# Kernel tuning notes

Hardware: AMD Instinct MI355X
Metric: run time of the kernel (lower is better)

The kernel has to match this reference:

```python
import jax, jax.numpy as jnp
import numpy as np

B, NP, NR = 4, 2048, 10
EDGE_F = 32
EMB = 64          # emb_features == out_features (required for layer stacking)
ESM_EMB = 64
HEADS = 16
NUM_LAYERS = 4
LN_EPS = 1e-5


def _ln(x, g, b):
    mu = jnp.mean(x, axis=-1, keepdims=True)
    var = jnp.var(x, axis=-1, keepdims=True)
    return (x - mu) / jnp.sqrt(var + LN_EPS) * g + b


def setup_inputs() -> dict:
    key = jax.random.key(0)
    ks = jax.random.split(key, 32)
    s = 0.05  # xavier-ish scale for weights
    inp = {
        "pep_feat": jax.random.normal(ks[0], (B, NP, 27 + 1280), jnp.float32),
        "rec_feat": jax.random.normal(ks[1], (B, NP, NR, 42 + 1280), jnp.float32),
        "edge_feat": jax.random.normal(ks[2], (B, NP, NR, EDGE_F), jnp.float32),
        # embedding weights (torch Linear convention: y = x @ W.T)
        "W_rec_esm": jax.random.normal(ks[3], (ESM_EMB, 1280), jnp.float32) * s,
        "W_pep_esm": jax.random.normal(ks[4], (ESM_EMB, 1280), jnp.float32) * s,
        "W_pep_emb": jax.random.normal(ks[5], (EMB, 27 + ESM_EMB), jnp.float32) * s,
        "W_rec_emb": jax.random.normal(ks[6], (EMB, 21 + ESM_EMB), jnp.float32) * s,
        "W_edge_emb": jax.random.normal(ks[7], (EMB, EDGE_F), jnp.float32) * s,
        "pep_ln_g": jnp.ones((EMB,), jnp.float32),
        "pep_ln_b": jnp.zeros((EMB,), jnp.float32),
        "rec_ln_g": jnp.ones((EMB,), jnp.float32),
        "rec_ln_b": jnp.zeros((EMB,), jnp.float32),
        # stacked GraphAttention layer params [L, ...]
        "ga_Wp": jax.random.normal(ks[8], (NUM_LAYERS, EMB, EMB), jnp.float32) * s,
        "ga_bp": jnp.zeros((NUM_LAYERS, EMB), jnp.float32),
        "ga_Wr": jax.random.normal(ks[9], (NUM_LAYERS, EMB, 2 * EMB), jnp.float32) * s,
        "ga_br": jnp.zeros((NUM_LAYERS, EMB), jnp.float32),
        "ga_Wv": jax.random.normal(ks[10], (NUM_LAYERS, EMB, 2 * EMB), jnp.float32) * s,
        "ga_bv": jnp.zeros((NUM_LAYERS, EMB), jnp.float32),
        # self-attention pooling: LN + MLP [64 -> 64 -> 32 -> 16 heads], no biases
        "pool_ln_g": jnp.ones((EMB,), jnp.float32),
        "pool_ln_b": jnp.zeros((EMB,), jnp.float32),
        "pool_W0": jax.random.normal(ks[11], (EMB, EMB), jnp.float32) * s,
        "pool_W1": jax.random.normal(ks[12], (EMB // 2, EMB), jnp.float32) * s,
        "pool_W2": jax.random.normal(ks[13], (HEADS, EMB // 2), jnp.float32) * s,
        # final projection
        "mlp_W": jax.random.normal(ks[14], (EMB // 2, EMB), jnp.float32) * s,
        "mlp_b": jnp.zeros((EMB // 2,), jnp.float32),
    }
    return inp


def _forward(pep_feat, rec_feat, edge_feat, W_rec_esm, W_pep_esm, W_pep_emb,
             W_rec_emb, W_edge_emb, pep_ln_g, pep_ln_b, rec_ln_g, rec_ln_b,
             ga_Wp, ga_bp, ga_Wr, ga_br, ga_Wv, ga_bv,
             pool_ln_g, pool_ln_b, pool_W0, pool_W1, pool_W2, mlp_W, mlp_b):
    # --- embeddings ---
    rec_esm = rec_feat[..., 42:] @ W_rec_esm.T                       # [B,NP,10,ESM]
    pep_esm = pep_feat[..., -1280:] @ W_pep_esm.T                    # [B,NP,ESM]
    rec = jnp.concatenate([rec_feat[..., :21], rec_esm], axis=-1) @ W_rec_emb.T
    pep = jnp.concatenate([pep_feat[..., :27], pep_esm], axis=-1) @ W_pep_emb.T
    edge = edge_feat @ W_edge_emb.T                                  # [B,NP,10,EMB]
    pep = _ln(pep, pep_ln_g, pep_ln_b)
    rec = _ln(rec, rec_ln_g, rec_ln_b)

    inv_sqrt_d = 1.0 / np.sqrt(EMB).astype(np.float32)
    rec_edge = jnp.concatenate([rec, edge], axis=-1)                 # [B,NP,10,2*EMB]
    # --- stacked GraphAttention layers (dropout = eval-mode identity) ---
    for l in range(NUM_LAYERS):
        q = pep @ ga_Wp[l].T + ga_bp[l]                              # [B,NP,EMB]
        key = rec_edge @ ga_Wr[l].T + ga_br[l]                       # [B,NP,10,EMB]
        val = rec_edge @ ga_Wv[l].T + ga_bv[l]                       # [B,NP,10,EMB]
        logit = jnp.einsum('bpd,bprd->bpr', q, key) * inv_sqrt_d     # [B,NP,10]
        attn = jax.nn.softmax(logit, axis=-1)
        pep = q + jnp.einsum('bpr,bprd->bpd', attn, val)             # [B,NP,EMB]

    # --- self-attention pooling (note: softmax applied twice, as in source) ---
    d = _ln(pep, pool_ln_g, pool_ln_b)                               # [B,NP,EMB]
    h = jnp.tanh(d @ pool_W0.T)
    h = jnp.tanh(h @ pool_W1.T)
    logits = h @ pool_W2.T                                           # [B,NP,HEADS]
    a = jax.nn.softmax(logits, axis=1)
    a = jax.nn.softmax(a, axis=1)
    attended = jnp.einsum('bsh,bsd->bhd', a, d)                      # [B,HEADS,EMB]
    pooled = attended.mean(axis=1)                                   # [B,EMB]
    return pooled @ mlp_W.T + mlp_b                                  # [B,EMB//2]


def reference(pep_feat, rec_feat, edge_feat, W_rec_esm, W_pep_esm, W_pep_emb,
              W_rec_emb, W_edge_emb, pep_ln_g, pep_ln_b, rec_ln_g, rec_ln_b,
              ga_Wp, ga_bp, ga_Wr, ga_br, ga_Wv, ga_bv,
              pool_ln_g, pool_ln_b, pool_W0, pool_W1, pool_W2, mlp_W, mlp_b):
    return _forward(pep_feat, rec_feat, edge_feat, W_rec_esm, W_pep_esm, W_pep_emb,
                    W_rec_emb, W_edge_emb, pep_ln_g, pep_ln_b, rec_ln_g, rec_ln_b,
                    ga_Wp, ga_bp, ga_Wr, ga_br, ga_Wv, ga_bv,
                    pool_ln_g, pool_ln_b, pool_W0, pool_W1, pool_W2, mlp_W, mlp_b)
```

## Files before the change

### kernel.cpp

```cpp
#include <hip/hip_runtime.h>
#include <hip/hip_bf16.h>


typedef __attribute__((ext_vector_type(8))) short bf16x8;
typedef __attribute__((ext_vector_type(4))) float f32x4;

#define MFMA(a, b, c) __builtin_amdgcn_mfma_f32_16x16x32_bf16((a), (b), (c), 0, 0, 0)

#define WB_REC_OFF   0
#define WB_PEP_OFF   83968
#define WB_EDGE_OFF  167936
#define WB_P_OFF     169984
#define WB_R_OFF     186368
#define WB_V_OFF     219136
#define WB_W0_OFF    251904
#define WB_W1_OFF    256000
#define WB_W2_OFF    258048
#define WB_TOTAL     258560

__device__ __forceinline__ unsigned short f2bf(float x) {
  __hip_bfloat16 h = __float2bfloat16(x);
  return __builtin_bit_cast(unsigned short, h);
}
__device__ __forceinline__ float bf2f(unsigned short u) {
  unsigned int t = ((unsigned int)u) << 16;
  return __builtin_bit_cast(float, t);
}
__device__ __forceinline__ bf16x8 loadBc(const unsigned short* base, int chunk, int lane) {
  return *(const bf16x8*)(base + ((size_t)chunk * 64 + lane) * 8);
}
__device__ __forceinline__ float tanhf_fast(float x) {
  float e = __expf(2.f * x);
  return 1.f - 2.f / (e + 1.f);
}
__device__ __forceinline__ int swzr(int r) {
  return (r & 1) | (((r >> 1) & 7) << 2);
}

__global__ __launch_bounds__(256) void k_pack(
    const float* __restrict__ Wresm, const float* __restrict__ Wpesm,
    const float* __restrict__ Wre, const float* __restrict__ Wpe,
    const float* __restrict__ Wedge, const float* __restrict__ Wp,
    const float* __restrict__ Wr, const float* __restrict__ Wv,
    const float* __restrict__ W0, const float* __restrict__ W1,
    const float* __restrict__ W2, unsigned short* __restrict__ WB) {
  const int t = blockIdx.x * 256 + threadIdx.x;
  if (t >= WB_TOTAL) return;
  float v = 0.f;
  if (t < WB_EDGE_OFF) {
    bool isPep = (t >= WB_PEP_OFF);
    int u = isPep ? (t - WB_PEP_OFF) : t;
    int j = u & 7, lane = (u >> 3) & 63, n = (u >> 9) & 3, kc = u >> 11;
    int k = kc * 32 + ((lane >> 4) << 3) + j;
    int col = n * 16 + (lane & 15);
    if (kc < 40) {
      const float* wemb = isPep ? (Wpe + col * 91 + 27) : (Wre + col * 85 + 21);
      const float* wesm = isPep ? Wpesm : Wresm;
      float s = 0.f;
#pragma unroll 8
      for (int e = 0; e < 64; ++e) s += wemb[e] * wesm[e * 1280 + k];
      v = s;
    } else {
      int kl = k - 1280;
      if (isPep) v = (kl < 27) ? Wpe[col * 91 + kl] : 0.f;
      else       v = (kl < 21) ? Wre[col * 85 + kl] : 0.f;
    }
  } else if (t < WB_P_OFF) {
    int u = t - WB_EDGE_OFF;
    int j = u & 7, lane = (u >> 3) & 63, n = (u >> 9) & 3;
    v = Wedge[(n * 16 + (lane & 15)) * 32 + ((lane >> 4) << 3) + j];
  } else if (t < WB_R_OFF) {
    int u = t - WB_P_OFF;
    int l = u >> 12, w = u & 4095;
    int j = w & 7, lane = (w >> 3) & 63, n = (w >> 9) & 3, kc = w >> 11;
    int o = kc * 32 + ((lane >> 4) << 3) + j;
    int d = n * 16 + (lane & 15);
    v = Wp[l * 4096 + d * 64 + o];
  } else if (t < WB_V_OFF) {
    int u = t - WB_R_OFF;
    int l = u >> 13, w = u & 8191;
    int j = w & 7, lane = (w >> 3) & 63, c = (w >> 9) & 15;
    int kc = c >> 3, n = c & 7;
    int o = kc * 32 + ((lane >> 4) << 3) + j;
    int k = n * 16 + (lane & 15);
    v = Wr[l * 8192 + o * 128 + k];
  } else if (t < WB_W0_OFF) {
    int u = t - WB_V_OFF;
    int l = u >> 13, w = u & 8191;
    int j = w & 7, lane = (w >> 3) & 63, n = (w >> 9) & 3, kc = w >> 11;
    int k = kc * 32 + ((lane >> 4) << 3) + j;
    int d = n * 16 + (lane & 15);
    v = Wv[l * 8192 + d * 128 + k];
  } else if (t < WB_W1_OFF) {
    int u = t - WB_W0_OFF;
    int j = u & 7, lane = (u >> 3) & 63, c = u >> 9;
    int kc = c >> 2, n = c & 3;
    v = W0[(n * 16 + (lane & 15)) * 64 + kc * 32 + ((lane >> 4) << 3) + j];
  } else if (t < WB_W2_OFF) {
    int u = t - WB_W1_OFF;
    int j = u & 7, lane = (u >> 3) & 63, c = u >> 9;
    int kc = c >> 1, n = c & 1;
    v = W1[(n * 16 + (lane & 15)) * 64 + kc * 32 + ((lane >> 4) << 3) + j];
  } else {
    int u = t - WB_W2_OFF;
    int j = u & 7, lane = (u >> 3) & 63;
    v = W2[(lane & 15) * 32 + ((lane >> 4) << 3) + j];
  }
  WB[t] = f2bf(v);
}

__global__ __launch_bounds__(64) void k_emb(
    const float* __restrict__ rec_feat, const float* __restrict__ edge_feat,
    const float* __restrict__ pep_feat, const unsigned short* __restrict__ WB,
    const float* __restrict__ rec_g, const float* __restrict__ rec_b,
    const float* __restrict__ pep_g, const float* __restrict__ pep_b,
    unsigned short* __restrict__ rec_edge, unsigned short* __restrict__ pep_out) {
  __shared__ float stg[2][16][128];
  const int bid = blockIdx.x;
  const int lane = threadIdx.x;
  const int quad = lane >> 4, lr = lane & 15;
  const bool isPep = (bid >= 5120);
  const int brow = (isPep ? bid - 5120 : bid) * 16;

  const f32x4 fz = {0.f, 0.f, 0.f, 0.f};
  f32x4 acc[4] = {fz, fz, fz, fz};

  auto frag = [&](int buf, int c) -> bf16x8 {
    const int u0 = c * 8 + quad * 2;
    const int s0 = u0 ^ swzr(lr), s1 = (u0 + 1) ^ swzr(lr);
    const float4 f0 = *(const float4*)((const char*)&stg[buf][lr][0] + s0 * 16);
    const float4 f1 = *(const float4*)((const char*)&stg[buf][lr][0] + s1 * 16);
    bf16x8 a;
#pragma unroll
    for (int j = 0; j < 4; ++j) { a[j] = (short)f2bf(f0[j]); a[4 + j] = (short)f2bf(f1[j]); }
    return a;
  };

  if (!isPep) {
    const float* base = rec_feat + (size_t)brow * 1322 + 42;
    float2 ld2[16];
    auto loadg = [&](int g) {
#pragma unroll
      for (int i = 0; i < 16; ++i)
        ld2[i] = *(const float2*)(base + (size_t)i * 1322 + g * 128 + lane * 2);
    };
    auto writeg = [&](int b) {
#pragma unroll
      for (int i = 0; i < 16; ++i) {
        const int su = (lane >> 1) ^ swzr(i);
        *(float2*)((char*)&stg[b][i][0] + su * 16 + (lane & 1) * 8) = ld2[i];
      }
    };
    loadg(0); writeg(0);
    int buf = 0;
    for (int g = 0; g < 10; ++g) {
      bf16x8 bb[16];
#pragma unroll
      for (int m = 0; m < 16; ++m) bb[m] = loadBc(WB + WB_REC_OFF, g * 16 + m, lane);
      if (g < 9) loadg(g + 1);
#pragma unroll
      for (int c = 0; c < 4; ++c) {
        const bf16x8 a = frag(buf, c);
#pragma unroll
        for (int n = 0; n < 4; ++n) acc[n] = MFMA(a, bb[c * 4 + n], acc[n]);
      }
      if (g < 9) writeg(buf ^ 1);
      buf ^= 1;
    }
    {
      const float* p = rec_feat + (size_t)(brow + lr) * 1322 + quad * 8;
      bf16x8 a;
#pragma unroll
      for (int m = 0; m < 4; ++m) {
        const float2 v = *(const float2*)(p + 2 * m);
        a[2 * m] = (short)f2bf(v.x); a[2 * m + 1] = (short)f2bf(v.y);
      }
#pragma unroll
      for (int n = 0; n < 4; ++n)
        acc[n] = MFMA(a, loadBc(WB + WB_REC_OFF, 160 + n, lane), acc[n]);
    }
  } else {
    const float* base = pep_feat + (size_t)brow * 1307 + 27;
    float ldp[32];
    auto loadg = [&](int g) {
#pragma unroll
      for (int i = 0; i < 16; ++i)
#pragma unroll
        for (int ph = 0; ph < 2; ++ph)
          ldp[i * 2 + ph] = base[(size_t)i * 1307 + g * 128 + ph * 64 + lane];
    };
    auto writeg = [&](int b) {
#pragma unroll
      for (int i = 0; i < 16; ++i)
#pragma unroll
        for (int ph = 0; ph < 2; ++ph) {
          const int su = (ph * 16 + (lane >> 2)) ^ swzr(i);
          *((float*)((char*)&stg[b][i][0] + su * 16 + (lane & 3) * 4)) = ldp[i * 2 + ph];
        }
    };
    loadg(0); writeg(0);
    int buf = 0;
    for (int g = 0; g < 10; ++g) {
      bf16x8 bb[16];
#pragma unroll
      for (int m = 0; m < 16; ++m) bb[m] = loadBc(WB + WB_PEP_OFF, g * 16 + m, lane);
      if (g < 9) loadg(g + 1);
#pragma unroll
      for (int c = 0; c < 4; ++c) {
        const bf16x8 a = frag(buf, c);
#pragma unroll
        for (int n = 0; n < 4; ++n) acc[n] = MFMA(a, bb[c * 4 + n], acc[n]);
      }
      if (g < 9) writeg(buf ^ 1);
      buf ^= 1;
    }
    {
      const float* p = pep_feat + (size_t)(brow + lr) * 1307 + quad * 8;
      bf16x8 a;
#pragma unroll
      for (int j = 0; j < 8; ++j) a[j] = (short)f2bf(p[j]);
#pragma unroll
      for (int n = 0; n < 4; ++n)
        acc[n] = MFMA(a, loadBc(WB + WB_PEP_OFF, 160 + n, lane), acc[n]);
    }
  }

  float s[4], sq[4];
#pragma unroll
  for (int i = 0; i < 4; ++i) {
    s[i] = acc[0][i] + acc[1][i] + acc[2][i] + acc[3][i];
    sq[i] = acc[0][i] * acc[0][i] + acc[1][i] * acc[1][i] +
            acc[2][i] * acc[2][i] + acc[3][i] * acc[3][i];
  }
#pragma unroll
  for (int msk = 1; msk < 16; msk <<= 1) {
#pragma unroll
    for (int i = 0; i < 4; ++i) {
      s[i] += __shfl_xor(s[i], msk);
      sq[i] += __shfl_xor(sq[i], msk);
    }
  }
  const float* gp = isPep ? pep_g : rec_g;
  const float* bp = isPep ? pep_b : rec_b;
  float gv[4], bvl[4];
#pragma unroll
  for (int n = 0; n < 4; ++n) { gv[n] = gp[lr + 16 * n]; bvl[n] = bp[lr + 16 * n]; }

  if (!isPep) {
    f32x4 acce[4] = {fz, fz, fz, fz};
    {
      const float* p = edge_feat + (size_t)(brow + lr) * 32 + quad * 8;
      const float4 f0 = *(const float4*)(p);
      const float4 f1 = *(const float4*)(p + 4);
      bf16x8 a;
#pragma unroll
      for (int j = 0; j < 4; ++j) { a[j] = (short)f2bf(f0[j]); a[4 + j] = (short)f2bf(f1[j]); }
#pragma unroll
      for (int n = 0; n < 4; ++n) acce[n] = MFMA(a, loadBc(WB + WB_EDGE_OFF, n, lane), acce[n]);
    }
#pragma unroll
    for (int i = 0; i < 4; ++i) {
      const float mean = s[i] * (1.f / 64.f);
      const float var = sq[i] * (1.f / 64.f) - mean * mean;
      const float rstd = rsqrtf(var + 1e-5f);
      unsigned short* dst = rec_edge + (size_t)(brow + quad * 4 + i) * 128;
#pragma unroll
      for (int n = 0; n < 4; ++n) {
        dst[lr + 16 * n] = f2bf((acc[n][i] - mean) * rstd * gv[n] + bvl[n]);
        dst[64 + lr + 16 * n] = f2bf(acce[n][i]);
      }
    }
  } else {
#pragma unroll
    for (int i = 0; i < 4; ++i) {
      const float mean = s[i] * (1.f / 64.f);
      const float var = sq[i] * (1.f / 64.f) - mean * mean;
      const float rstd = rsqrtf(var + 1e-5f);
      unsigned short* dst = pep_out + (size_t)(brow + quad * 4 + i) * 64;
#pragma unroll
      for (int n = 0; n < 4; ++n)
        dst[lr + 16 * n] = f2bf((acc[n][i] - mean) * rstd * gv[n] + bvl[n]);
    }
  }
}

__global__ __launch_bounds__(64) void k_ga(
    const unsigned short* __restrict__ rec_edge, const unsigned short* __restrict__ pep_bf,
    const unsigned short* __restrict__ WB,
    const float* __restrict__ ga_bp, const float* __restrict__ ga_bv,
    const float* __restrict__ pool_g, const float* __restrict__ pool_b,
    float* __restrict__ dbuf, float* __restrict__ logitsT) {
  __shared__ unsigned short pep_s[1024];
  __shared__ unsigned short q_s[1024];
  __shared__ unsigned short zs[2048];
  __shared__ float bias_s[512];

  const int lane = threadIdx.x;
  const int quad = lane >> 4, lr = lane & 15;
  const int swz = lr & 7;
  const int pbase = blockIdx.x * 16;
  const f32x4 fz = {0.f, 0.f, 0.f, 0.f};

#pragma unroll
  for (int i = 0; i < 4; ++i) {
    int f = lane + 64 * i;
    bias_s[f] = ga_bp[f];
    bias_s[256 + f] = ga_bv[f];
  }
#pragma unroll
  for (int i = 0; i < 2; ++i) {
    const int G = lane + 64 * i;
    const int p = G >> 3, gg = G & 7;
    const bf16x8 v = *(const bf16x8*)(pep_bf + (size_t)(pbase + p) * 64 + gg * 8);
    *(bf16x8*)(pep_s + p * 64 + ((gg ^ (p & 7)) << 3)) = v;
  }

  auto bwrite = [&](unsigned short* buf, int p, int col, unsigned short val) {
    buf[p * 64 + ((((col >> 3)) ^ (p & 7)) << 3) + (col & 7)] = val;
  };
  auto bfrag = [&](const unsigned short* buf, int kc) -> bf16x8 {
    return *(const bf16x8*)(buf + lr * 64 + ((((kc << 2) + quad) ^ swz) << 3));
  };
  const unsigned short* reb = rec_edge + (size_t)(pbase + lr) * 1280 + quad * 8;

  f32x4 pcur[4];
  for (int l = 0; l < 4; ++l) {
    const unsigned short* WBp = WB + WB_P_OFF + l * 4096;
    const unsigned short* WBr = WB + WB_R_OFF + l * 8192;
    const unsigned short* WBv = WB + WB_V_OFF + l * 8192;
    f32x4 qa[4] = {fz, fz, fz, fz};
#pragma unroll
    for (int kc = 0; kc < 2; ++kc) {
      bf16x8 a = bfrag(pep_s, kc);
#pragma unroll
      for (int n = 0; n < 4; ++n) qa[n] = MFMA(a, loadBc(WBp, kc * 4 + n, lane), qa[n]);
    }
#pragma unroll
    for (int n = 0; n < 4; ++n) {
      const float bpv = bias_s[l * 64 + lr + 16 * n];
#pragma unroll
      for (int i = 0; i < 4; ++i) qa[n][i] += bpv;
    }
#pragma unroll
    for (int n = 0; n < 4; ++n)
#pragma unroll
      for (int i = 0; i < 4; ++i)
        bwrite(q_s, quad * 4 + i, lr + 16 * n, f2bf(qa[n][i]));
    const bf16x8 aq0 = bfrag(q_s, 0), aq1 = bfrag(q_s, 1);
    f32x4 za[8] = {fz, fz, fz, fz, fz, fz, fz, fz};
#pragma unroll
    for (int n = 0; n < 8; ++n) za[n] = MFMA(aq0, loadBc(WBr, n, lane), za[n]);
#pragma unroll
    for (int n = 0; n < 8; ++n) za[n] = MFMA(aq1, loadBc(WBr, 8 + n, lane), za[n]);
#pragma unroll
    for (int n = 0; n < 8; ++n)
#pragma unroll
      for (int i = 0; i < 4; ++i) {
        const int p = quad * 4 + i, k = 16 * n + lr;
        zs[p * 128 + ((((k >> 3) ^ (p & 7)) << 3) | (k & 7))] = f2bf(za[n][i]);
      }
    float zf[4][8];
#pragma unroll
    for (int kc = 0; kc < 4; ++kc) {
      const bf16x8 z8 = *(const bf16x8*)(zs + lr * 128 + (((quad + 4 * kc) ^ swz) << 3));
#pragma unroll
      for (int j = 0; j < 8; ++j) zf[kc][j] = bf2f((unsigned short)z8[j]);
    }
    float lg[10];
#pragma unroll 2
    for (int r = 0; r < 10; ++r) {
      float part = 0.f;
#pragma unroll
      for (int kc = 0; kc < 4; ++kc) {
        const bf16x8 rf = *(const bf16x8*)(reb + r * 128 + kc * 32);
#pragma unroll
        for (int j = 0; j < 8; ++j) part += bf2f((unsigned short)rf[j]) * zf[kc][j];
      }
      part += __shfl_xor(part, 16);
      part += __shfl_xor(part, 32);
      lg[r] = part * 0.125f;
    }
    float mx = lg[0];
#pragma unroll
    for (int r = 1; r < 10; ++r) mx = fmaxf(mx, lg[r]);
    float ssum = 0.f;
#pragma unroll
    for (int r = 0; r < 10; ++r) { lg[r] = __expf(lg[r] - mx); ssum += lg[r]; }
    const float inv = 1.f / ssum;
#pragma unroll
    for (int r = 0; r < 10; ++r) lg[r] *= inv;
    float wsacc[4][8] = {};
#pragma unroll 2
    for (int r = 0; r < 10; ++r) {
#pragma unroll
      for (int kc = 0; kc < 4; ++kc) {
        const bf16x8 rf = *(const bf16x8*)(reb + r * 128 + kc * 32);
#pragma unroll
        for (int j = 0; j < 8; ++j)
          wsacc[kc][j] += lg[r] * bf2f((unsigned short)rf[j]);
      }
    }
    bf16x8 wf[4];
#pragma unroll
    for (int kc = 0; kc < 4; ++kc)
#pragma unroll
      for (int j = 0; j < 8; ++j) wf[kc][j] = (short)f2bf(wsacc[kc][j]);
    f32x4 oa[4] = {fz, fz, fz, fz};
#pragma unroll
    for (int kc = 0; kc < 4; ++kc)
#pragma unroll
      for (int n = 0; n < 4; ++n) oa[n] = MFMA(wf[kc], loadBc(WBv, kc * 4 + n, lane), oa[n]);
#pragma unroll
    for (int n = 0; n < 4; ++n) {
      const float bvv = bias_s[256 + l * 64 + lr + 16 * n];
#pragma unroll
      for (int i = 0; i < 4; ++i) pcur[n][i] = qa[n][i] + oa[n][i] + bvv;
    }
#pragma unroll
    for (int n = 0; n < 4; ++n)
#pragma unroll
      for (int i = 0; i < 4; ++i)
        bwrite(pep_s, quad * 4 + i, lr + 16 * n, f2bf(pcur[n][i]));
  }

  {
    float s[4], sq[4];
#pragma unroll
    for (int i = 0; i < 4; ++i) {
      s[i] = pcur[0][i] + pcur[1][i] + pcur[2][i] + pcur[3][i];
      sq[i] = pcur[0][i] * pcur[0][i] + pcur[1][i] * pcur[1][i] +
              pcur[2][i] * pcur[2][i] + pcur[3][i] * pcur[3][i];
    }
#pragma unroll
    for (int msk = 1; msk < 16; msk <<= 1) {
#pragma unroll
      for (int i = 0; i < 4; ++i) {
        s[i] += __shfl_xor(s[i], msk);
        sq[i] += __shfl_xor(sq[i], msk);
      }
    }
    float gv[4], bv2[4];
#pragma unroll
    for (int n = 0; n < 4; ++n) { gv[n] = pool_g[lr + 16 * n]; bv2[n] = pool_b[lr + 16 * n]; }
    f32x4 d[4];
#pragma unroll
    for (int i = 0; i < 4; ++i) {
      const float mean = s[i] * (1.f / 64.f);
      const float var = sq[i] * (1.f / 64.f) - mean * mean;
      const float rstd = rsqrtf(var + 1e-5f);
#pragma unroll
      for (int n = 0; n < 4; ++n) d[n][i] = (pcur[n][i] - mean) * rstd * gv[n] + bv2[n];
    }
    float* zf32 = (float*)zs;
#pragma unroll
    for (int n = 0; n < 4; ++n)
#pragma unroll
      for (int i = 0; i < 4; ++i)
        zf32[(quad * 4 + i) * 64 + lr + 16 * n] = d[n][i];
#pragma unroll
    for (int i = 0; i < 4; ++i) {
      const float4 v = *(const float4*)(&zf32[i * 256 + lane * 4]);
      *(float4*)(dbuf + (size_t)pbase * 64 + i * 256 + lane * 4) = v;
    }
#pragma unroll
    for (int n = 0; n < 4; ++n)
#pragma unroll
      for (int i = 0; i < 4; ++i)
        bwrite(q_s, quad * 4 + i, lr + 16 * n, f2bf(d[n][i]));
    const bf16x8 ad0 = bfrag(q_s, 0), ad1 = bfrag(q_s, 1);
    f32x4 h0[4] = {fz, fz, fz, fz};
#pragma unroll
    for (int n = 0; n < 4; ++n) {
      h0[n] = MFMA(ad0, loadBc(WB + WB_W0_OFF, n, lane), h0[n]);
      h0[n] = MFMA(ad1, loadBc(WB + WB_W0_OFF, 4 + n, lane), h0[n]);
    }
#pragma unroll
    for (int n = 0; n < 4; ++n)
#pragma unroll
      for (int i = 0; i < 4; ++i)
        bwrite(q_s, quad * 4 + i, lr + 16 * n, f2bf(tanhf_fast(h0[n][i])));
    const bf16x8 ah00 = bfrag(q_s, 0), ah01 = bfrag(q_s, 1);
    f32x4 h1[2] = {fz, fz};
#pragma unroll
    for (int n = 0; n < 2; ++n) {
      h1[n] = MFMA(ah00, loadBc(WB + WB_W1_OFF, n, lane), h1[n]);
      h1[n] = MFMA(ah01, loadBc(WB + WB_W1_OFF, 2 + n, lane), h1[n]);
    }
#pragma unroll
    for (int n = 0; n < 2; ++n)
#pragma unroll
      for (int i = 0; i < 4; ++i)
        bwrite(q_s, quad * 4 + i, lr + 16 * n, f2bf(tanhf_fast(h1[n][i])));
    const bf16x8 ah1 = bfrag(q_s, 0);
    f32x4 lac = MFMA(ah1, loadBc(WB + WB_W2_OFF, 0, lane), fz);
    const int b = pbase >> 11, sx0 = pbase & 2047;
#pragma unroll
    for (int i = 0; i < 4; ++i)
      logitsT[(size_t)(b * 16 + lr) * 2048 + sx0 + quad * 4 + i] = lac[i];
  }
}

__global__ __launch_bounds__(256) void k_pool2(
    const float* __restrict__ logitsT, const float* __restrict__ dbuf,
    float* __restrict__ attp) {
  __shared__ float sh[2048];
  __shared__ float red[8];
  __shared__ float part[16][64];
  const int blk = blockIdx.x;
  const int bh = blk >> 2, q = blk & 3;
  const int b = bh >> 4;
  const int tid = threadIdx.x, lane = tid & 63, wid = tid >> 6;
  const float* lrow = logitsT + (size_t)bh * 2048;

  float m = -1e30f;
  for (int sx = tid; sx < 2048; sx += 256) {
    float v = lrow[sx];
    sh[sx] = v;
    m = fmaxf(m, v);
  }
#pragma unroll
  for (int msk = 1; msk < 64; msk <<= 1) m = fmaxf(m, __shfl_xor(m, msk));
  if (lane == 0) red[wid] = m;
  __syncthreads();
  m = fmaxf(fmaxf(red[0], red[1]), fmaxf(red[2], red[3]));

  float s1 = 0.f;
  for (int sx = tid; sx < 2048; sx += 256) {
    float e = __expf(sh[sx] - m);
    sh[sx] = e;
    s1 += e;
  }
#pragma unroll
  for (int msk = 1; msk < 64; msk <<= 1) s1 += __shfl_xor(s1, msk);
  __syncthreads();
  if (lane == 0) red[4 + wid] = s1;
  __syncthreads();
  s1 = red[4] + red[5] + red[6] + red[7];
  const float invS1 = 1.f / s1;

  float s2 = 0.f;
  for (int sx = tid; sx < 2048; sx += 256) {
    float e2 = __expf((sh[sx] - 1.f) * invS1);
    sh[sx] = e2;
    s2 += e2;
  }
#pragma unroll
  for (int msk = 1; msk < 64; msk <<= 1) s2 += __shfl_xor(s2, msk);
  __syncthreads();
  if (lane == 0) red[wid] = s2;
  __syncthreads();
  s2 = red[0] + red[1] + red[2] + red[3];
  const float invS2 = 1.f / s2;

  const int d16 = tid & 15, sxg = tid >> 4;
  float4 a4 = {0.f, 0.f, 0.f, 0.f};
  const float* db = dbuf + (size_t)b * 2048 * 64 + d16 * 4;
#pragma unroll 4
  for (int sx = q * 512 + sxg; sx < (q + 1) * 512; sx += 16) {
    const float w = sh[sx];
    const float4 v = *(const float4*)(db + (size_t)sx * 64);
    a4.x += w * v.x; a4.y += w * v.y; a4.z += w * v.z; a4.w += w * v.w;
  }
  *(float4*)(&part[sxg][d16 * 4]) = a4;
  __syncthreads();
  if (tid < 64) {
    float s = 0.f;
#pragma unroll
    for (int g2 = 0; g2 < 16; ++g2) s += part[g2][tid];
    attp[(size_t)(bh * 4 + q) * 64 + tid] = s * invS2;
  }
}

__global__ __launch_bounds__(256) void k_final(
    const float* __restrict__ attp, const float* __restrict__ W,
    const float* __restrict__ bias, float* __restrict__ out) {
  __shared__ float pooled[4][64];
  const int tid = threadIdx.x;
  {
    const int b = tid >> 6, d = tid & 63;
    float s = 0.f;
#pragma unroll
    for (int hq = 0; hq < 64; ++hq) s += attp[((size_t)b * 64 + hq) * 64 + d];
    pooled[b][d] = s * (1.f / 16.f);
  }
  __syncthreads();
  if (tid < 128) {
    const int b = tid >> 5, j = tid & 31;
    float s = bias[j];
#pragma unroll
    for (int d2 = 0; d2 < 64; ++d2) s += pooled[b][d2] * W[j * 64 + d2];
    out[b * 32 + j] = s;
  }
}

extern "C" void kernel_launch(void* const* d_in, const int* in_sizes, int n_in,
                              void* d_out, int out_size, void* d_ws, size_t ws_size,
                              hipStream_t stream) {
  const float* pep_feat = (const float*)d_in[0];
  const float* rec_feat = (const float*)d_in[1];
  const float* edge_feat = (const float*)d_in[2];
  const float* W_rec_esm = (const float*)d_in[3];
  const float* W_pep_esm = (const float*)d_in[4];
  const float* W_pep_emb = (const float*)d_in[5];
  const float* W_rec_emb = (const float*)d_in[6];
  const float* W_edge_emb = (const float*)d_in[7];
  const float* pep_ln_g = (const float*)d_in[8];
  const float* pep_ln_b = (const float*)d_in[9];
  const float* rec_ln_g = (const float*)d_in[10];
  const float* rec_ln_b = (const float*)d_in[11];
  const float* ga_Wp = (const float*)d_in[12];
  const float* ga_bp = (const float*)d_in[13];
  const float* ga_Wr = (const float*)d_in[14];
  const float* ga_br = (const float*)d_in[15];
  const float* ga_Wv = (const float*)d_in[16];
  const float* ga_bv = (const float*)d_in[17];
  const float* pool_ln_g = (const float*)d_in[18];
  const float* pool_ln_b = (const float*)d_in[19];
  const float* pool_W0 = (const float*)d_in[20];
  const float* pool_W1 = (const float*)d_in[21];
  const float* pool_W2 = (const float*)d_in[22];
  const float* mlp_W = (const float*)d_in[23];
  const float* mlp_b = (const float*)d_in[24];
  float* out = (float*)d_out;
  (void)ga_br;
  (void)ws_size; (void)in_sizes; (void)n_in; (void)out_size;

  char* ws = (char*)d_ws;
  unsigned short* WB = (unsigned short*)(ws);
  unsigned short* rec_edge = (unsigned short*)(ws + 524288);
  unsigned short* pep_bf = (unsigned short*)(ws + 21495808);
  float* dbuf = (float*)(ws + 22544384);
  float* logitsT = (float*)(ws + 24641536);
  float* attp = (float*)(ws + 25165824);

  k_pack<<<1010, 256, 0, stream>>>(W_rec_esm, W_pep_esm, W_rec_emb, W_pep_emb,
                                   W_edge_emb, ga_Wp, ga_Wr, ga_Wv,
                                   pool_W0, pool_W1, pool_W2, WB);
  k_emb<<<5632, 64, 0, stream>>>(rec_feat, edge_feat, pep_feat, WB,
                                 rec_ln_g, rec_ln_b, pep_ln_g, pep_ln_b,
                                 rec_edge, pep_bf);
  k_ga<<<512, 64, 0, stream>>>(rec_edge, pep_bf, WB, ga_bp, ga_bv,
                               pool_ln_g, pool_ln_b, dbuf, logitsT);
  k_pool2<<<256, 256, 0, stream>>>(logitsT, dbuf, attp);
  k_final<<<1, 256, 0, stream>>>(attp, mlp_W, mlp_b, out);
}
```

Measured before the change: 190.9 us.

## Split graph-attention kernel across four waves per 16-peptide block

```diff
diff --git a/kernel.cpp b/kernel.cpp
--- a/kernel.cpp
+++ b/kernel.cpp
@@ -284,7 +284,7 @@
   }
 }
 
-__global__ __launch_bounds__(64) void k_ga(
+__global__ __launch_bounds__(256) void k_ga(
     const unsigned short* __restrict__ rec_edge, const unsigned short* __restrict__ pep_bf,
     const unsigned short* __restrict__ WB,
     const float* __restrict__ ga_bp, const float* __restrict__ ga_bv,
@@ -292,28 +292,34 @@
     float* __restrict__ dbuf, float* __restrict__ logitsT) {
   __shared__ unsigned short pep_s[1024];
   __shared__ unsigned short q_s[1024];
-  __shared__ unsigned short zs[2048];
+  __shared__ __align__(16) unsigned short zs[2048];
   __shared__ float bias_s[512];
-
-  const int lane = threadIdx.x;
+  __shared__ float lgp[4][10][17];
+  __shared__ float redp[4][2][16];
+  __shared__ float oap[4][16][68];
+
+  const int tid = threadIdx.x;
+  const int w = tid >> 6;
+  const int lane = tid & 63;
   const int quad = lane >> 4, lr = lane & 15;
   const int swz = lr & 7;
   const int pbase = blockIdx.x * 16;
+  const int mycol = lr + 16 * w;
   const f32x4 fz = {0.f, 0.f, 0.f, 0.f};
 
-#pragma unroll
-  for (int i = 0; i < 4; ++i) {
-    int f = lane + 64 * i;
-    bias_s[f] = ga_bp[f];
-    bias_s[256 + f] = ga_bv[f];
-  }
-#pragma unroll
-  for (int i = 0; i < 2; ++i) {
-    const int G = lane + 64 * i;
-    const int p = G >> 3, gg = G & 7;
+  bias_s[tid] = ga_bp[tid & 255];
+  bias_s[256 + tid] = ga_bv[tid & 255];
+  if (tid < 128) {
+    const int p = tid >> 3, gg = tid & 7;
     const bf16x8 v = *(const bf16x8*)(pep_bf + (size_t)(pbase + p) * 64 + gg * 8);
     *(bf16x8*)(pep_s + p * 64 + ((gg ^ (p & 7)) << 3)) = v;
   }
+  const unsigned short* reb =
+      rec_edge + (size_t)(pbase + lr) * 1280 + w * 32 + quad * 8;
+  bf16x8 rfs[10];
+#pragma unroll
+  for (int r = 0; r < 10; ++r) rfs[r] = *(const bf16x8*)(reb + r * 128);
+  __syncthreads();
 
   auto bwrite = [&](unsigned short* buf, int p, int col, unsigned short val) {
     buf[p * 64 + ((((col >> 3)) ^ (p & 7)) << 3) + (col & 7)] = val;
@@ -321,65 +327,56 @@
   auto bfrag = [&](const unsigned short* buf, int kc) -> bf16x8 {
     return *(const bf16x8*)(buf + lr * 64 + ((((kc << 2) + quad) ^ swz) << 3));
   };
-  const unsigned short* reb = rec_edge + (size_t)(pbase + lr) * 1280 + quad * 8;
-
-  f32x4 pcur[4];
+
+  f32x4 pcur;
   for (int l = 0; l < 4; ++l) {
     const unsigned short* WBp = WB + WB_P_OFF + l * 4096;
     const unsigned short* WBr = WB + WB_R_OFF + l * 8192;
     const unsigned short* WBv = WB + WB_V_OFF + l * 8192;
-    f32x4 qa[4] = {fz, fz, fz, fz};
-#pragma unroll
-    for (int kc = 0; kc < 2; ++kc) {
-      bf16x8 a = bfrag(pep_s, kc);
-#pragma unroll
-      for (int n = 0; n < 4; ++n) qa[n] = MFMA(a, loadBc(WBp, kc * 4 + n, lane), qa[n]);
-    }
-#pragma unroll
-    for (int n = 0; n < 4; ++n) {
-      const float bpv = bias_s[l * 64 + lr + 16 * n];
-#pragma unroll
-      for (int i = 0; i < 4; ++i) qa[n][i] += bpv;
-    }
-#pragma unroll
-    for (int n = 0; n < 4; ++n)
-#pragma unroll
-      for (int i = 0; i < 4; ++i)
-        bwrite(q_s, quad * 4 + i, lr + 16 * n, f2bf(qa[n][i]));
+
+    f32x4 qa = fz;
+    qa = MFMA(bfrag(pep_s, 0), loadBc(WBp, w, lane), qa);
+    qa = MFMA(bfrag(pep_s, 1), loadBc(WBp, 4 + w, lane), qa);
+    const float bpv = bias_s[l * 64 + mycol];
+#pragma unroll
+    for (int i = 0; i < 4; ++i) qa[i] += bpv;
+#pragma unroll
+    for (int i = 0; i < 4; ++i) bwrite(q_s, quad * 4 + i, mycol, f2bf(qa[i]));
+    __syncthreads();
+
     const bf16x8 aq0 = bfrag(q_s, 0), aq1 = bfrag(q_s, 1);
-    f32x4 za[8] = {fz, fz, fz, fz, fz, fz, fz, fz};
-#pragma unroll
-    for (int n = 0; n < 8; ++n) za[n] = MFMA(aq0, loadBc(WBr, n, lane), za[n]);
-#pragma unroll
-    for (int n = 0; n < 8; ++n) za[n] = MFMA(aq1, loadBc(WBr, 8 + n, lane), za[n]);
-#pragma unroll
-    for (int n = 0; n < 8; ++n)
-#pragma unroll
-      for (int i = 0; i < 4; ++i) {
-        const int p = quad * 4 + i, k = 16 * n + lr;
-        zs[p * 128 + ((((k >> 3) ^ (p & 7)) << 3) | (k & 7))] = f2bf(za[n][i]);
-      }
-    float zf[4][8];
-#pragma unroll
-    for (int kc = 0; kc < 4; ++kc) {
-      const bf16x8 z8 = *(const bf16x8*)(zs + lr * 128 + (((quad + 4 * kc) ^ swz) << 3));
-#pragma unroll
-      for (int j = 0; j < 8; ++j) zf[kc][j] = bf2f((unsigned short)z8[j]);
-    }
-    float lg[10];
-#pragma unroll 2
+    f32x4 za0 = fz, za1 = fz;
+    za0 = MFMA(aq0, loadBc(WBr, 2 * w, lane), za0);
+    za0 = MFMA(aq1, loadBc(WBr, 8 + 2 * w, lane), za0);
+    za1 = MFMA(aq0, loadBc(WBr, 2 * w + 1, lane), za1);
+    za1 = MFMA(aq1, loadBc(WBr, 9 + 2 * w, lane), za1);
+#pragma unroll
+    for (int i = 0; i < 4; ++i) {
+      const int p = quad * 4 + i;
+      const int k0 = 16 * (2 * w) + lr, k1 = 16 * (2 * w + 1) + lr;
+      zs[p * 128 + ((((k0 >> 3) ^ (p & 7)) << 3) | (k0 & 7))] = f2bf(za0[i]);
+      zs[p * 128 + ((((k1 >> 3) ^ (p & 7)) << 3) | (k1 & 7))] = f2bf(za1[i]);
+    }
+    float zfw[8];
+    {
+      const bf16x8 z8 = *(const bf16x8*)(zs + lr * 128 + (((quad + 4 * w) ^ swz) << 3));
+#pragma unroll
+      for (int j = 0; j < 8; ++j) zfw[j] = bf2f((unsigned short)z8[j]);
+    }
+#pragma unroll
     for (int r = 0; r < 10; ++r) {
       float part = 0.f;
 #pragma unroll
-      for (int kc = 0; kc < 4; ++kc) {
-        const bf16x8 rf = *(const bf16x8*)(reb + r * 128 + kc * 32);
-#pragma unroll
-        for (int j = 0; j < 8; ++j) part += bf2f((unsigned short)rf[j]) * zf[kc][j];
-      }
+      for (int j = 0; j < 8; ++j) part += bf2f((unsigned short)rfs[r][j]) * zfw[j];
       part += __shfl_xor(part, 16);
       part += __shfl_xor(part, 32);
-      lg[r] = part * 0.125f;
-    }
+      if (quad == 0) lgp[w][r][lr] = part;
+    }
+    __syncthreads();
+    float lg[10];
+#pragma unroll
+    for (int r = 0; r < 10; ++r)
+      lg[r] = (lgp[0][r][lr] + lgp[1][r][lr] + lgp[2][r][lr] + lgp[3][r][lr]) * 0.125f;
     float mx = lg[0];
 #pragma unroll
     for (int r = 1; r < 10; ++r) mx = fmaxf(mx, lg[r]);
@@ -389,48 +386,41 @@
     const float inv = 1.f / ssum;
 #pragma unroll
     for (int r = 0; r < 10; ++r) lg[r] *= inv;
-    float wsacc[4][8] = {};
-#pragma unroll 2
-    for (int r = 0; r < 10; ++r) {
-#pragma unroll
-      for (int kc = 0; kc < 4; ++kc) {
-        const bf16x8 rf = *(const bf16x8*)(reb + r * 128 + kc * 32);
-#pragma unroll
-        for (int j = 0; j < 8; ++j)
-          wsacc[kc][j] += lg[r] * bf2f((unsigned short)rf[j]);
-      }
-    }
-    bf16x8 wf[4];
-#pragma unroll
-    for (int kc = 0; kc < 4; ++kc)
-#pragma unroll
-      for (int j = 0; j < 8; ++j) wf[kc][j] = (short)f2bf(wsacc[kc][j]);
-    f32x4 oa[4] = {fz, fz, fz, fz};
-#pragma unroll
-    for (int kc = 0; kc < 4; ++kc)
-#pragma unroll
-      for (int n = 0; n < 4; ++n) oa[n] = MFMA(wf[kc], loadBc(WBv, kc * 4 + n, lane), oa[n]);
-#pragma unroll
-    for (int n = 0; n < 4; ++n) {
-      const float bvv = bias_s[256 + l * 64 + lr + 16 * n];
-#pragma unroll
-      for (int i = 0; i < 4; ++i) pcur[n][i] = qa[n][i] + oa[n][i] + bvv;
-    }
+    float wsacc[8] = {};
+#pragma unroll
+    for (int r = 0; r < 10; ++r)
+#pragma unroll
+      for (int j = 0; j < 8; ++j)
+        wsacc[j] += lg[r] * bf2f((unsigned short)rfs[r][j]);
+    bf16x8 wf;
+#pragma unroll
+    for (int j = 0; j < 8; ++j) wf[j] = (short)f2bf(wsacc[j]);
+    f32x4 oa[4];
+#pragma unroll
+    for (int n = 0; n < 4; ++n) oa[n] = MFMA(wf, loadBc(WBv, w * 4 + n, lane), fz);
 #pragma unroll
     for (int n = 0; n < 4; ++n)
 #pragma unroll
       for (int i = 0; i < 4; ++i)
-        bwrite(pep_s, quad * 4 + i, lr + 16 * n, f2bf(pcur[n][i]));
+        oap[w][quad * 4 + i][n * 16 + lr] = oa[n][i];
+    __syncthreads();
+    const float bvv = bias_s[256 + l * 64 + mycol];
+#pragma unroll
+    for (int i = 0; i < 4; ++i) {
+      const int p = quad * 4 + i;
+      const float o = oap[0][p][mycol] + oap[1][p][mycol] +
+                      oap[2][p][mycol] + oap[3][p][mycol];
+      pcur[i] = qa[i] + o + bvv;
+    }
+#pragma unroll
+    for (int i = 0; i < 4; ++i) bwrite(pep_s, quad * 4 + i, mycol, f2bf(pcur[i]));
+    __syncthreads();
   }
 
   {
     float s[4], sq[4];
 #pragma unroll
-    for (int i = 0; i < 4; ++i) {
-      s[i] = pcur[0][i] + pcur[1][i] + pcur[2][i] + pcur[3][i];
-      sq[i] = pcur[0][i] * pcur[0][i] + pcur[1][i] * pcur[1][i] +
-              pcur[2][i] * pcur[2][i] + pcur[3][i] * pcur[3][i];
-    }
+    for (int i = 0; i < 4; ++i) { s[i] = pcur[i]; sq[i] = pcur[i] * pcur[i]; }
 #pragma unroll
     for (int msk = 1; msk < 16; msk <<= 1) {
 #pragma unroll
@@ -439,64 +429,66 @@
         sq[i] += __shfl_xor(sq[i], msk);
       }
     }
-    float gv[4], bv2[4];
-#pragma unroll
-    for (int n = 0; n < 4; ++n) { gv[n] = pool_g[lr + 16 * n]; bv2[n] = pool_b[lr + 16 * n]; }
-    f32x4 d[4];
+    if (lr == 0) {
+#pragma unroll
+      for (int i = 0; i < 4; ++i) {
+        redp[w][0][quad * 4 + i] = s[i];
+        redp[w][1][quad * 4 + i] = sq[i];
+      }
+    }
+    __syncthreads();
+    const float gv = pool_g[mycol], bv2 = pool_b[mycol];
+    float d[4];
+    float* zf32 = (float*)zs;
 #pragma unroll
     for (int i = 0; i < 4; ++i) {
-      const float mean = s[i] * (1.f / 64.f);
-      const float var = sq[i] * (1.f / 64.f) - mean * mean;
+      const int p = quad * 4 + i;
+      const float sf = redp[0][0][p] + redp[1][0][p] + redp[2][0][p] + redp[3][0][p];
+      const float sqf = redp[0][1][p] + redp[1][1][p] + redp[2][1][p] + redp[3][1][p];
+      const float mean = sf * (1.f / 64.f);
+      const float var = sqf * (1.f / 64.f) - mean * mean;
       const float rstd = rsqrtf(var + 1e-5f);
-#pragma unroll
-      for (int n = 0; n < 4; ++n) d[n][i] = (pcur[n][i] - mean) * rstd * gv[n] + bv2[n];
-    }
-    float* zf32 = (float*)zs;
-#pragma unroll
-    for (int n = 0; n < 4; ++n)
+      d[i] = (pcur[i] - mean) * rstd * gv + bv2;
+      zf32[p * 64 + mycol] = d[i];
+      bwrite(q_s, p, mycol, f2bf(d[i]));
+    }
+    __syncthreads();
+    {
+      const float4 v = *(const float4*)(&zf32[tid * 4]);
+      *(float4*)(dbuf + (size_t)pbase * 64 + tid * 4) = v;
+    }
+    if (w == 0) {
+      const bf16x8 ad0 = bfrag(q_s, 0), ad1 = bfrag(q_s, 1);
+      f32x4 h0[4] = {fz, fz, fz, fz};
+#pragma unroll
+      for (int n = 0; n < 4; ++n) {
+        h0[n] = MFMA(ad0, loadBc(WB + WB_W0_OFF, n, lane), h0[n]);
+        h0[n] = MFMA(ad1, loadBc(WB + WB_W0_OFF, 4 + n, lane), h0[n]);
+      }
+#pragma unroll
+      for (int n = 0; n < 4; ++n)
+#pragma unroll
+        for (int i = 0; i < 4; ++i)
+          bwrite(q_s, quad * 4 + i, lr + 16 * n, f2bf(tanhf_fast(h0[n][i])));
+      const bf16x8 ah00 = bfrag(q_s, 0), ah01 = bfrag(q_s, 1);
+      f32x4 h1[2] = {fz, fz};
+#pragma unroll
+      for (int n = 0; n < 2; ++n) {
+        h1[n] = MFMA(ah00, loadBc(WB + WB_W1_OFF, n, lane), h1[n]);
+        h1[n] = MFMA(ah01, loadBc(WB + WB_W1_OFF, 2 + n, lane), h1[n]);
+      }
+#pragma unroll
+      for (int n = 0; n < 2; ++n)
+#pragma unroll
+        for (int i = 0; i < 4; ++i)
+          bwrite(q_s, quad * 4 + i, lr + 16 * n, f2bf(tanhf_fast(h1[n][i])));
+      const bf16x8 ah1 = bfrag(q_s, 0);
+      f32x4 lac = MFMA(ah1, loadBc(WB + WB_W2_OFF, 0, lane), fz);
+      const int b = pbase >> 11, sx0 = pbase & 2047;
 #pragma unroll
       for (int i = 0; i < 4; ++i)
-        zf32[(quad * 4 + i) * 64 + lr + 16 * n] = d[n][i];
-#pragma unroll
-    for (int i = 0; i < 4; ++i) {
-      const float4 v = *(const float4*)(&zf32[i * 256 + lane * 4]);
-      *(float4*)(dbuf + (size_t)pbase * 64 + i * 256 + lane * 4) = v;
-    }
-#pragma unroll
-    for (int n = 0; n < 4; ++n)
-#pragma unroll
-      for (int i = 0; i < 4; ++i)
-        bwrite(q_s, quad * 4 + i, lr + 16 * n, f2bf(d[n][i]));
-    const bf16x8 ad0 = bfrag(q_s, 0), ad1 = bfrag(q_s, 1);
-    f32x4 h0[4] = {fz, fz, fz, fz};
-#pragma unroll
-    for (int n = 0; n < 4; ++n) {
-      h0[n] = MFMA(ad0, loadBc(WB + WB_W0_OFF, n, lane), h0[n]);
-      h0[n] = MFMA(ad1, loadBc(WB + WB_W0_OFF, 4 + n, lane), h0[n]);
-    }
-#pragma unroll
-    for (int n = 0; n < 4; ++n)
-#pragma unroll
-      for (int i = 0; i < 4; ++i)
-        bwrite(q_s, quad * 4 + i, lr + 16 * n, f2bf(tanhf_fast(h0[n][i])));
-    const bf16x8 ah00 = bfrag(q_s, 0), ah01 = bfrag(q_s, 1);
-    f32x4 h1[2] = {fz, fz};
-#pragma unroll
-    for (int n = 0; n < 2; ++n) {
-      h1[n] = MFMA(ah00, loadBc(WB + WB_W1_OFF, n, lane), h1[n]);
-      h1[n] = MFMA(ah01, loadBc(WB + WB_W1_OFF, 2 + n, lane), h1[n]);
-    }
-#pragma unroll
-    for (int n = 0; n < 2; ++n)
-#pragma unroll
-      for (int i = 0; i < 4; ++i)
-        bwrite(q_s, quad * 4 + i, lr + 16 * n, f2bf(tanhf_fast(h1[n][i])));
-    const bf16x8 ah1 = bfrag(q_s, 0);
-    f32x4 lac = MFMA(ah1, loadBc(WB + WB_W2_OFF, 0, lane), fz);
-    const int b = pbase >> 11, sx0 = pbase & 2047;
-#pragma unroll
-    for (int i = 0; i < 4; ++i)
-      logitsT[(size_t)(b * 16 + lr) * 2048 + sx0 + quad * 4 + i] = lac[i];
+        logitsT[(size_t)(b * 16 + lr) * 2048 + sx0 + quad * 4 + i] = lac[i];
+    }
   }
 }
 
@@ -639,8 +631,8 @@
   k_emb<<<5632, 64, 0, stream>>>(rec_feat, edge_feat, pep_feat, WB,
                                  rec_ln_g, rec_ln_b, pep_ln_g, pep_ln_b,
                                  rec_edge, pep_bf);
-  k_ga<<<512, 64, 0, stream>>>(rec_edge, pep_bf, WB, ga_bp, ga_bv,
-                               pool_ln_g, pool_ln_b, dbuf, logitsT);
+  k_ga<<<512, 256, 0, stream>>>(rec_edge, pep_bf, WB, ga_bp, ga_bv,
+                                pool_ln_g, pool_ln_b, dbuf, logitsT);
   k_pool2<<<256, 256, 0, stream>>>(logitsT, dbuf, attp);
   k_final<<<1, 256, 0, stream>>>(attp, mlp_W, mlp_b, out);
 }
```

After: 170.3 us. 1.12x faster.
